# Kernel optimization log

Measured on AMD Instinct MI355X. Metric: run time of the kernel, lower is better.

## Reference

```python
import jax, jax.numpy as jnp
import numpy as np


def setup_inputs() -> dict:
    key = jax.random.key(0)
    ks = jax.random.split(key, 8)
    B, C, H, W = 4, 512, 64, 64
    C8 = C // 8
    return {
        "x": jax.random.normal(ks[0], (B, C, H, W), dtype=jnp.float32),
        "Wq": jax.random.normal(ks[1], (C8, C), dtype=jnp.float32) * 0.02,
        "bq": jax.random.normal(ks[2], (C8,), dtype=jnp.float32) * 0.02,
        "Wk": jax.random.normal(ks[3], (C8, C), dtype=jnp.float32) * 0.02,
        "bk": jax.random.normal(ks[4], (C8,), dtype=jnp.float32) * 0.02,
        "Wv": jax.random.normal(ks[5], (C, C), dtype=jnp.float32) * 0.02,
        "bv": jax.random.normal(ks[6], (C,), dtype=jnp.float32) * 0.02,
        "gamma": jax.random.normal(ks[7], (1,), dtype=jnp.float32),
    }


def reference(x, Wq, bq, Wk, bk, Wv, bv, gamma):
    B, C, H, W = x.shape
    N = H * W
    xf = x.reshape(B, C, N)  # 1x1 conv == per-position matmul over channels
    q = jnp.einsum('oc,bcn->bno', Wq, xf) + bq  # B, N, C//8  (proj_query^T)
    k = jnp.einsum('oc,bcn->bon', Wk, xf) + bk[None, :, None]  # B, C//8, N
    v = jnp.einsum('oc,bcn->bon', Wv, xf) + bv[None, :, None]  # B, C, N
    energy = jnp.einsum('bno,bom->bnm', q, k)  # B, N, N
    attention = jax.nn.softmax(energy, axis=-1)
    # out = bmm(proj_value, attention^T): out[:, :, n] = sum_m v[:, :, m] * att[n, m]
    out = jnp.einsum('bcm,bnm->bcn', v, attention).reshape(B, C, H, W)
    return gamma[0] * out + x
```

## Files before the change

kernel.cpp:

```cpp
#include <hip/hip_runtime.h>
#include <stdint.h>


typedef unsigned short u16;
typedef unsigned char u8;
typedef __attribute__((ext_vector_type(8))) short short8;
typedef __attribute__((ext_vector_type(4))) float f32x4;
typedef __attribute__((ext_vector_type(16))) float f32x16;
typedef __attribute__((ext_vector_type(4))) int i32x4;
typedef __attribute__((ext_vector_type(8))) int i32x8;

#define ASYNC16(gp, lp)                                                        \
  __builtin_amdgcn_global_load_lds(                                            \
      (__attribute__((address_space(1))) void*)(void*)(gp),                    \
      (__attribute__((address_space(3))) void*)(lp), 16, 0, 0)

#define WAIT_VM0 0x0F70
#define WAIT_VM3 0x0F73
#define WAIT_LGKM0 0xC07F

#define EXP_SHIFT 5.0f
#define EXP_CAP 57000.0f

__device__ __forceinline__ u16 f2bf(float f) {
  uint32_t u = __float_as_uint(f);
  u += 0x7FFFu + ((u >> 16) & 1u);
  return (u16)(u >> 16);
}

__device__ __forceinline__ u8 f2fp8(float f) {
  f = fminf(fmaxf(f, -440.f), 440.f);
  int r = __builtin_amdgcn_cvt_pk_fp8_f32(f, f, 0, false);
  return (u8)(r & 0xFF);
}

__global__ __launch_bounds__(256) void k_transpose(const float* __restrict__ x,
                                                   u16* __restrict__ xT) {
  __shared__ float tile[64][65];
  const int b = blockIdx.z;
  const int nb = blockIdx.x * 64;
  const int cb = blockIdx.y * 64;
  const int t = threadIdx.x;
  {
    const int nl = (t & 15) * 4, c0 = t >> 4;
    const float* xp = x + ((size_t)b * 512 + cb) * 4096 + nb;
#pragma unroll
    for (int p = 0; p < 4; ++p) {
      const int cl = c0 + p * 16;
      const float4 v = *(const float4*)(xp + (size_t)cl * 4096 + nl);
      tile[cl][nl] = v.x;
      tile[cl][nl + 1] = v.y;
      tile[cl][nl + 2] = v.z;
      tile[cl][nl + 3] = v.w;
    }
  }
  __syncthreads();
  {
    const int cl = (t & 15) * 4, n0 = t >> 4;
    u16* xtp = xT + ((size_t)b * 4096 + nb) * 512 + cb;
#pragma unroll
    for (int p = 0; p < 4; ++p) {
      const int nl = n0 + p * 16;
      ushort4 o;
      o.x = f2bf(tile[cl][nl]);
      o.y = f2bf(tile[cl + 1][nl]);
      o.z = f2bf(tile[cl + 2][nl]);
      o.w = f2bf(tile[cl + 3][nl]);
      *(ushort4*)(xtp + (size_t)nl * 512 + cl) = o;
    }
  }
}

__global__ __launch_bounds__(256) void k_wcast(const float* __restrict__ Wq,
                                               const float* __restrict__ Wk,
                                               const float* __restrict__ Wv,
                                               u16* __restrict__ wqk,
                                               u16* __restrict__ wv) {
  const int idx = blockIdx.x * 256 + threadIdx.x;
  if (idx < 128 * 512) {
    const int r = idx >> 9, c = idx & 511;
    const float f = (r < 64) ? Wq[r * 512 + c] : Wk[(r - 64) * 512 + c];
    wqk[idx] = f2bf(f);
  } else {
    const int j = idx - 128 * 512;
    if (j < 512 * 512) wv[j] = f2bf(Wv[j]);
  }
}

__device__ __forceinline__ void gemm_bt_tile(const u16* __restrict__ A,
                                             const u16* __restrict__ B,
                                             const int K, const int rowA0,
                                             const int colB0, u16* smem,
                                             f32x4 acc[4][4]) {
  const int t = threadIdx.x;
  const int lane = t & 63, wave = t >> 6;
  const int quad = lane >> 4, l15 = lane & 15;
  const int wr = wave >> 1, wc = wave & 1;
  u16* As = smem;
  u16* Bs = smem + 8192;
  const f32x4 zero = {0.f, 0.f, 0.f, 0.f};
#pragma unroll
  for (int i = 0; i < 4; ++i)
#pragma unroll
    for (int j = 0; j < 4; ++j) acc[i][j] = zero;

  const int srow = t >> 3;
  const int c8 = (lane & 7) ^ (lane >> 3);
  const u16* ga = A + (size_t)(rowA0 + srow) * K + c8 * 8;
  const u16* gb = B + (size_t)(colB0 + srow) * K + c8 * 8;
  char* la = (char*)As + wave * 1024;
  char* lb = (char*)Bs + wave * 1024;
  const size_t rK32 = (size_t)32 * K;

  const int sw0 = (quad) ^ (l15 & 7);
  const int sw1 = (4 + quad) ^ (l15 & 7);

  for (int k0 = 0; k0 < K; k0 += 64) {
    ASYNC16(ga + k0, la);
    ASYNC16(ga + k0 + rK32, la + 4096);
    ASYNC16(ga + k0 + 2 * rK32, la + 8192);
    ASYNC16(ga + k0 + 3 * rK32, la + 12288);
    ASYNC16(gb + k0, lb);
    ASYNC16(gb + k0 + rK32, lb + 4096);
    ASYNC16(gb + k0 + 2 * rK32, lb + 8192);
    ASYNC16(gb + k0 + 3 * rK32, lb + 12288);
    __syncthreads();
#pragma unroll
    for (int s = 0; s < 2; ++s) {
      const int sw = s ? sw1 : sw0;
      short8 a[4], b[4];
#pragma unroll
      for (int i = 0; i < 4; ++i)
        a[i] = *(const short8*)(As + (wr * 64 + i * 16 + l15) * 64 + sw * 8);
#pragma unroll
      for (int j = 0; j < 4; ++j)
        b[j] = *(const short8*)(Bs + (wc * 64 + j * 16 + l15) * 64 + sw * 8);
#pragma unroll
      for (int i = 0; i < 4; ++i)
#pragma unroll
        for (int j = 0; j < 4; ++j)
          acc[i][j] = __builtin_amdgcn_mfma_f32_16x16x32_bf16(a[i], b[j],
                                                              acc[i][j], 0, 0, 0);
    }
    __syncthreads();
  }
}

__global__ __launch_bounds__(256) void k_proj(const u16* __restrict__ xT,
                                              const u16* __restrict__ wqk,
                                              const u16* __restrict__ wv,
                                              const float* __restrict__ bq,
                                              const float* __restrict__ bk,
                                              const float* __restrict__ bv,
                                              u16* __restrict__ q,
                                              u16* __restrict__ kT,
                                              u8* __restrict__ v8) {
  __shared__ u16 smem[16384];
  const int b = blockIdx.z;
  const int by = blockIdx.y;
  const int t = threadIdx.x, lane = t & 63, wave = t >> 6;
  const int quad = lane >> 4, l15 = lane & 15;
  const int wr = wave >> 1, wc = wave & 1;
  f32x4 acc[4][4];

  if (by == 4) {
    const int rowA0 = blockIdx.x * 128;
    gemm_bt_tile(xT + (size_t)b * 4096 * 512, wqk, 512, rowA0, 0, smem, acc);
#pragma unroll
    for (int j = 0; j < 4; ++j) {
      const int col = wc * 64 + j * 16 + l15;
      const float bias = (col < 64) ? bq[col] : bk[col - 64];
#pragma unroll
      for (int i = 0; i < 4; ++i) {
#pragma unroll
        for (int r = 0; r < 4; ++r) {
          const int row = rowA0 + wr * 64 + i * 16 + quad * 4 + r;
          const float val = acc[i][j][r] + bias;
          if (col < 64)
            q[((size_t)b * 4096 + row) * 64 + col] = f2bf(val);
          else
            kT[((size_t)b * 4096 + row) * 64 + (col - 64)] = f2bf(val);
        }
      }
    }
  } else {
    const int rowA0 = by * 128;
    const int colB0 = blockIdx.x * 128;
    gemm_bt_tile(wv, xT + (size_t)b * 4096 * 512, 512, rowA0, colB0, smem, acc);
#pragma unroll
    for (int i = 0; i < 4; ++i) {
#pragma unroll
      for (int r = 0; r < 4; ++r) {
        const int row = rowA0 + wr * 64 + i * 16 + quad * 4 + r;
        const float bias = bv[row];
#pragma unroll
        for (int j = 0; j < 4; ++j) {
          const int col = colB0 + wc * 64 + j * 16 + l15;
          v8[((size_t)b * 512 + row) * 4096 + col] = f2fp8(acc[i][j][r] + bias);
        }
      }
    }
  }
}

__global__ __launch_bounds__(1024, 4) void k_fused(
    const u16* __restrict__ q, const u16* __restrict__ kT,
    const u8* __restrict__ v8, const float* __restrict__ x,
    const float* __restrict__ gamma, float* __restrict__ out) {
  __shared__ u16 k_lds[2][128 * 64];
  __shared__ u8 v_lds[2][2][256 * 64];
  __shared__ u8 P_lds[2][128 * 64];
  __shared__ float lsum_lds[8][128];

  const int t = threadIdx.x;
  const int l = t & 63, w = t >> 6;
  const int quad = l >> 4, l15 = l & 15;
  const int l31 = l & 31, h = l >> 5;

  const int n0 = blockIdx.x * 128;
  const int c0 = blockIdx.y * 256;
  const int b = blockIdx.z;

  const u16* qg = q + ((size_t)b * 4096 + n0) * 64;
  const u16* kg = kT + (size_t)b * 4096 * 64;
  const u8* vg = v8 + ((size_t)b * 512 + c0) * 4096;

  const int kr = t >> 3, kc = t & 7;
  const u16* qsg = qg + kr * 64 + (kc ^ (kr & 7)) * 8;
  const u16* ksg = kg + kr * 64 + (kc ^ (kr & 7)) * 8;
  const int vr = t >> 2, va = t & 3;
  const u8* vsg = vg + (size_t)vr * 4096 + (va ^ ((vr >> 1) & 3)) * 16;

#define STAGE_F(bi, m0)                                                        \
  do {                                                                         \
    ASYNC16(ksg + (size_t)(m0) * 64, (char*)k_lds[bi] + w * 1024);             \
    ASYNC16(vsg + (m0), (char*)v_lds[bi][0] + w * 1024);                       \
    ASYNC16(vsg + (m0) + 64, (char*)v_lds[bi][1] + w * 1024);                  \
  } while (0)

  ASYNC16(qsg, (char*)P_lds[0] + w * 1024);
  STAGE_F(0, 0);
  __builtin_amdgcn_s_waitcnt(WAIT_VM3);
  __builtin_amdgcn_s_barrier();
  asm volatile("" ::: "memory");
  const int ms = w >> 1, nh = w & 1;
  const int sw0 = quad ^ (l15 & 7);
  const int sw1 = (4 + quad) ^ (l15 & 7);
  short8 af[4][2];
#pragma unroll
  for (int s = 0; s < 4; ++s) {
    const u16* qrow = (const u16*)P_lds[0] + (nh * 64 + s * 16 + l15) * 64;
    af[s][0] = *(const short8*)(qrow + sw0 * 8);
    af[s][1] = *(const short8*)(qrow + sw1 * 8);
  }
  asm volatile("" ::: "memory");
  __builtin_amdgcn_s_waitcnt(WAIT_LGKM0);
  __builtin_amdgcn_s_barrier();
  asm volatile("" ::: "memory");

  const int wrp = w >> 2, wcp = w & 3;
  int rowA[2], sA1[2], sA2[2];
#pragma unroll
  for (int i = 0; i < 2; ++i) {
    rowA[i] = wrp * 64 + i * 32 + l31;
    const int fa = (rowA[i] >> 1) & 3;
    sA1[i] = (2 * h) ^ fa;
    sA2[i] = (2 * h + 1) ^ fa;
  }
  const int rowB = wcp * 32 + l31;
  const int fbB = (rowB >> 1) & 3;
  const int sB1 = (2 * h) ^ fbB;
  const int sB2 = (2 * h + 1) ^ fbB;

  const int fbW = (l15 >> 1) & 3;
  u8* Pwbase = P_lds[ms >> 2] + (nh * 64 + l15) * 64 +
               (((ms & 3) ^ fbW) * 16) + quad * 4;

  const int krow_off = (ms * 16 + l15) * 64;

  f32x16 acc[2];
#pragma unroll
  for (int i = 0; i < 2; ++i)
#pragma unroll
    for (int r = 0; r < 16; ++r) acc[i][r] = 0.f;

  float lsums[4] = {0.f, 0.f, 0.f, 0.f};
  const f32x4 zero = {0.f, 0.f, 0.f, 0.f};

  for (int it = 0; it < 32; ++it) {
    __builtin_amdgcn_s_waitcnt(WAIT_VM0);
    asm volatile("" ::: "memory");
    __builtin_amdgcn_s_barrier();
    asm volatile("" ::: "memory");
    const int cur = it & 1;
    if (it + 1 < 32) STAGE_F(cur ^ 1, (it + 1) * 128);

    const u16* kb = k_lds[cur];
    const short8 kf0 = *(const short8*)(kb + krow_off + sw0 * 8);
    const short8 kf1 = *(const short8*)(kb + krow_off + sw1 * 8);
    f32x4 eacc[4];
#pragma unroll
    for (int s = 0; s < 4; ++s) eacc[s] = zero;
    __builtin_amdgcn_s_setprio(1);
#pragma unroll
    for (int s = 0; s < 4; ++s)
      eacc[s] = __builtin_amdgcn_mfma_f32_16x16x32_bf16(kf0, af[s][0],
                                                        eacc[s], 0, 0, 0);
#pragma unroll
    for (int s = 0; s < 4; ++s)
      eacc[s] = __builtin_amdgcn_mfma_f32_16x16x32_bf16(kf1, af[s][1],
                                                        eacc[s], 0, 0, 0);
    __builtin_amdgcn_s_setprio(0);

#pragma unroll
    for (int s = 0; s < 4; ++s) {
      const float e0 = fminf(__expf(eacc[s][0] - EXP_SHIFT), EXP_CAP);
      const float e1 = fminf(__expf(eacc[s][1] - EXP_SHIFT), EXP_CAP);
      const float e2 = fminf(__expf(eacc[s][2] - EXP_SHIFT), EXP_CAP);
      const float e3 = fminf(__expf(eacc[s][3] - EXP_SHIFT), EXP_CAP);
      lsums[s] += (e0 + e1) + (e2 + e3);
      int pk = __builtin_amdgcn_cvt_pk_bf8_f32(e0, e1, 0, false);
      pk = __builtin_amdgcn_cvt_pk_bf8_f32(e2, e3, pk, true);
      *(int*)(Pwbase + s * 1024) = pk;
    }
    asm volatile("" ::: "memory");
    __builtin_amdgcn_s_waitcnt(WAIT_LGKM0);
    __builtin_amdgcn_s_barrier();
    asm volatile("" ::: "memory");

#pragma unroll
    for (int ks = 0; ks < 2; ++ks) {
      const u8* Vb = v_lds[cur][ks];
      const u8* Pb = P_lds[ks];
      i32x8 bb;
      {
        const u8* pb = Pb + rowB * 64;
        const i32x4 blo = *(const i32x4*)(pb + sB1 * 16);
        const i32x4 bhi = *(const i32x4*)(pb + sB2 * 16);
        bb[0] = blo[0]; bb[1] = blo[1]; bb[2] = blo[2]; bb[3] = blo[3];
        bb[4] = bhi[0]; bb[5] = bhi[1]; bb[6] = bhi[2]; bb[7] = bhi[3];
      }
      __builtin_amdgcn_s_setprio(1);
#pragma unroll
      for (int i = 0; i < 2; ++i) {
        const u8* pa = Vb + rowA[i] * 64;
        const i32x4 lo = *(const i32x4*)(pa + sA1[i] * 16);
        const i32x4 hi = *(const i32x4*)(pa + sA2[i] * 16);
        i32x8 a;
        a[0] = lo[0]; a[1] = lo[1]; a[2] = lo[2]; a[3] = lo[3];
        a[4] = hi[0]; a[5] = hi[1]; a[6] = hi[2]; a[7] = hi[3];
        acc[i] = __builtin_amdgcn_mfma_scale_f32_32x32x64_f8f6f4(
            a, bb, acc[i], 0 , 1 , 0, 0x7F, 0, 0x7F);
      }
      __builtin_amdgcn_s_setprio(0);
    }
    asm volatile("" ::: "memory");
  }
#undef STAGE_F

#pragma unroll
  for (int s = 0; s < 4; ++s) {
    lsums[s] += __shfl_xor(lsums[s], 16);
    lsums[s] += __shfl_xor(lsums[s], 32);
  }
  if (l < 16) {
#pragma unroll
    for (int s = 0; s < 4; ++s)
      lsum_lds[ms][nh * 64 + s * 16 + l] = lsums[s];
  }
  asm volatile("" ::: "memory");
  __builtin_amdgcn_s_waitcnt(WAIT_LGKM0);
  __builtin_amdgcn_s_barrier();
  asm volatile("" ::: "memory");

  const float g = gamma[0];
  const int col = n0 + wcp * 32 + l31;
  const int nc = wcp * 32 + l31;
  float den = 0.f;
#pragma unroll
  for (int m = 0; m < 8; ++m) den += lsum_lds[m][nc];
  const float gil = g / den;
#pragma unroll
  for (int i = 0; i < 2; ++i) {
#pragma unroll
    for (int r = 0; r < 16; ++r) {
      const int rloc = (r & 3) + 8 * (r >> 2) + 4 * h;
      const int row = c0 + wrp * 64 + i * 32 + rloc;
      const size_t idx = ((size_t)b * 512 + row) * 4096 + col;
      out[idx] = gil * acc[i][r] + x[idx];
    }
  }
}

extern "C" void kernel_launch(void* const* d_in, const int* in_sizes, int n_in,
                              void* d_out, int out_size, void* d_ws,
                              size_t ws_size, hipStream_t stream) {
  const float* x = (const float*)d_in[0];
  const float* Wq = (const float*)d_in[1];
  const float* bq = (const float*)d_in[2];
  const float* Wk = (const float*)d_in[3];
  const float* bk = (const float*)d_in[4];
  const float* Wv = (const float*)d_in[5];
  const float* bv = (const float*)d_in[6];
  const float* gamma = (const float*)d_in[7];
  float* out = (float*)d_out;

  char* ws = (char*)d_ws;
  u16* xT = (u16*)(ws);
  u16* wqk = (u16*)(ws + 16777216);
  u16* wv = (u16*)(ws + 16908288);
  u16* qb = (u16*)(ws + 17432576);
  u16* ktb = (u16*)(ws + 19529728);
  u8* v8 = (u8*)(ws + 21626880);

  k_transpose<<<dim3(64, 8, 4), 256, 0, stream>>>(x, xT);
  k_wcast<<<dim3(1280), 256, 0, stream>>>(Wq, Wk, Wv, wqk, wv);
  k_proj<<<dim3(32, 5, 4), 256, 0, stream>>>(xT, wqk, wv, bq, bk, bv,
                                             qb, ktb, v8);
  k_fused<<<dim3(32, 2, 4), 1024, 0, stream>>>(qb, ktb, v8, x, gamma, out);
}
```

Baseline: 197.9 us.

## Double-buffer projection GEMM with 8 waves and async prefetch pipeline

The projection GEMM now runs with 512 threads (8 waves, each computing a 64x32 sub-tile) and a two-stage LDS double buffer. The next K-slices are issued with async global-to-LDS loads while MFMAs run on the current buffer, using a vmcnt wait instead of a full sync. MFMA sections are raised to priority 1 with s_setprio. The aim is to hide global load latency and raise occupancy in k_proj, at the cost of twice the LDS per block.

Result: faster. 189.8 us (-4.1%).

```diff
diff --git a/kernel.cpp b/kernel.cpp
--- a/kernel.cpp
+++ b/kernel.cpp
@@ -17,6 +17,7 @@
 
 #define WAIT_VM0 0x0F70
 #define WAIT_VM3 0x0F73
+#define WAIT_VM4 0x0F74
 #define WAIT_LGKM0 0xC07F
 
 #define EXP_SHIFT 5.0f
@@ -87,88 +88,105 @@
   }
 }
 
-__device__ __forceinline__ void gemm_bt_tile(const u16* __restrict__ A,
-                                             const u16* __restrict__ B,
-                                             const int K, const int rowA0,
-                                             const int colB0, u16* smem,
-                                             f32x4 acc[4][4]) {
+__device__ __forceinline__ void gemm8_bt(const u16* __restrict__ A,
+                                         const u16* __restrict__ B,
+                                         const int K, const int rowA0,
+                                         const int colB0, u16* smem,
+                                         f32x4 acc[4][2]) {
   const int t = threadIdx.x;
-  const int lane = t & 63, wave = t >> 6;
+  const int lane = t & 63, w = t >> 6;
   const int quad = lane >> 4, l15 = lane & 15;
-  const int wr = wave >> 1, wc = wave & 1;
-  u16* As = smem;
-  u16* Bs = smem + 8192;
+  const int wr = w >> 2, wc = w & 3;
   const f32x4 zero = {0.f, 0.f, 0.f, 0.f};
 #pragma unroll
   for (int i = 0; i < 4; ++i)
 #pragma unroll
-    for (int j = 0; j < 4; ++j) acc[i][j] = zero;
+    for (int j = 0; j < 2; ++j) acc[i][j] = zero;
 
   const int srow = t >> 3;
   const int c8 = (lane & 7) ^ (lane >> 3);
   const u16* ga = A + (size_t)(rowA0 + srow) * K + c8 * 8;
   const u16* gb = B + (size_t)(colB0 + srow) * K + c8 * 8;
-  char* la = (char*)As + wave * 1024;
-  char* lb = (char*)Bs + wave * 1024;
-  const size_t rK32 = (size_t)32 * K;
+  const size_t rK64 = (size_t)64 * K;
+
+#define STAGE_G(bi, k0)                                                        \
+  do {                                                                         \
+    char* Ab = (char*)smem + (bi) * 32768 + w * 1024;                          \
+    char* Bb = (char*)smem + (bi) * 32768 + 16384 + w * 1024;                  \
+    ASYNC16(ga + (k0), Ab);                                                    \
+    ASYNC16(ga + (k0) + rK64, Ab + 8192);                                      \
+    ASYNC16(gb + (k0), Bb);                                                    \
+    ASYNC16(gb + (k0) + rK64, Bb + 8192);                                      \
+  } while (0)
 
   const int sw0 = (quad) ^ (l15 & 7);
   const int sw1 = (4 + quad) ^ (l15 & 7);
 
-  for (int k0 = 0; k0 < K; k0 += 64) {
-    ASYNC16(ga + k0, la);
-    ASYNC16(ga + k0 + rK32, la + 4096);
-    ASYNC16(ga + k0 + 2 * rK32, la + 8192);
-    ASYNC16(ga + k0 + 3 * rK32, la + 12288);
-    ASYNC16(gb + k0, lb);
-    ASYNC16(gb + k0 + rK32, lb + 4096);
-    ASYNC16(gb + k0 + 2 * rK32, lb + 8192);
-    ASYNC16(gb + k0 + 3 * rK32, lb + 12288);
-    __syncthreads();
+  const int nIt = K >> 6;
+  STAGE_G(0, 0);
+  STAGE_G(1, 64);
+
+  for (int it = 0; it < nIt; ++it) {
+    if (it < nIt - 1)
+      __builtin_amdgcn_s_waitcnt(WAIT_VM4);
+    else
+      __builtin_amdgcn_s_waitcnt(WAIT_VM0);
+    asm volatile("" ::: "memory");
+    __builtin_amdgcn_s_barrier();
+    asm volatile("" ::: "memory");
+
+    const u16* As = smem + (it & 1) * 16384;
+    const u16* Bs = As + 8192;
 #pragma unroll
     for (int s = 0; s < 2; ++s) {
       const int sw = s ? sw1 : sw0;
-      short8 a[4], b[4];
+      short8 a[4], b[2];
 #pragma unroll
       for (int i = 0; i < 4; ++i)
         a[i] = *(const short8*)(As + (wr * 64 + i * 16 + l15) * 64 + sw * 8);
 #pragma unroll
-      for (int j = 0; j < 4; ++j)
-        b[j] = *(const short8*)(Bs + (wc * 64 + j * 16 + l15) * 64 + sw * 8);
+      for (int j = 0; j < 2; ++j)
+        b[j] = *(const short8*)(Bs + (wc * 32 + j * 16 + l15) * 64 + sw * 8);
+      __builtin_amdgcn_s_setprio(1);
 #pragma unroll
       for (int i = 0; i < 4; ++i)
 #pragma unroll
-        for (int j = 0; j < 4; ++j)
+        for (int j = 0; j < 2; ++j)
           acc[i][j] = __builtin_amdgcn_mfma_f32_16x16x32_bf16(a[i], b[j],
                                                               acc[i][j], 0, 0, 0);
-    }
-    __syncthreads();
-  }
-}
-
-__global__ __launch_bounds__(256) void k_proj(const u16* __restrict__ xT,
-                                              const u16* __restrict__ wqk,
-                                              const u16* __restrict__ wv,
-                                              const float* __restrict__ bq,
-                                              const float* __restrict__ bk,
-                                              const float* __restrict__ bv,
-                                              u16* __restrict__ q,
-                                              u16* __restrict__ kT,
-                                              u8* __restrict__ v8) {
-  __shared__ u16 smem[16384];
+      __builtin_amdgcn_s_setprio(0);
+    }
+    asm volatile("" ::: "memory");
+    __builtin_amdgcn_s_barrier();
+    asm volatile("" ::: "memory");
+    if (it + 2 < nIt) STAGE_G(it & 1, (it + 2) * 64);
+  }
+#undef STAGE_G
+}
+
+__global__ __launch_bounds__(512, 4) void k_proj(const u16* __restrict__ xT,
+                                                 const u16* __restrict__ wqk,
+                                                 const u16* __restrict__ wv,
+                                                 const float* __restrict__ bq,
+                                                 const float* __restrict__ bk,
+                                                 const float* __restrict__ bv,
+                                                 u16* __restrict__ q,
+                                                 u16* __restrict__ kT,
+                                                 u8* __restrict__ v8) {
+  __shared__ u16 smem[32768];
   const int b = blockIdx.z;
   const int by = blockIdx.y;
-  const int t = threadIdx.x, lane = t & 63, wave = t >> 6;
+  const int t = threadIdx.x, lane = t & 63, w = t >> 6;
   const int quad = lane >> 4, l15 = lane & 15;
-  const int wr = wave >> 1, wc = wave & 1;
-  f32x4 acc[4][4];
+  const int wr = w >> 2, wc = w & 3;
+  f32x4 acc[4][2];
 
   if (by == 4) {
     const int rowA0 = blockIdx.x * 128;
-    gemm_bt_tile(xT + (size_t)b * 4096 * 512, wqk, 512, rowA0, 0, smem, acc);
-#pragma unroll
-    for (int j = 0; j < 4; ++j) {
-      const int col = wc * 64 + j * 16 + l15;
+    gemm8_bt(xT + (size_t)b * 4096 * 512, wqk, 512, rowA0, 0, smem, acc);
+#pragma unroll
+    for (int j = 0; j < 2; ++j) {
+      const int col = wc * 32 + j * 16 + l15;
       const float bias = (col < 64) ? bq[col] : bk[col - 64];
 #pragma unroll
       for (int i = 0; i < 4; ++i) {
@@ -186,7 +204,7 @@
   } else {
     const int rowA0 = by * 128;
     const int colB0 = blockIdx.x * 128;
-    gemm_bt_tile(wv, xT + (size_t)b * 4096 * 512, 512, rowA0, colB0, smem, acc);
+    gemm8_bt(wv, xT + (size_t)b * 4096 * 512, 512, rowA0, colB0, smem, acc);
 #pragma unroll
     for (int i = 0; i < 4; ++i) {
 #pragma unroll
@@ -194,8 +212,8 @@
         const int row = rowA0 + wr * 64 + i * 16 + quad * 4 + r;
         const float bias = bv[row];
 #pragma unroll
-        for (int j = 0; j < 4; ++j) {
-          const int col = colB0 + wc * 64 + j * 16 + l15;
+        for (int j = 0; j < 2; ++j) {
+          const int col = colB0 + wc * 32 + j * 16 + l15;
           v8[((size_t)b * 512 + row) * 4096 + col] = f2fp8(acc[i][j][r] + bias);
         }
       }
@@ -415,7 +433,7 @@
 
   k_transpose<<<dim3(64, 8, 4), 256, 0, stream>>>(x, xT);
   k_wcast<<<dim3(1280), 256, 0, stream>>>(Wq, Wk, Wv, wqk, wv);
-  k_proj<<<dim3(32, 5, 4), 256, 0, stream>>>(xT, wqk, wv, bq, bk, bv,
+  k_proj<<<dim3(32, 5, 4), 512, 0, stream>>>(xT, wqk, wv, bq, bk, bv,
                                              qb, ktb, v8);
   k_fused<<<dim3(32, 2, 4), 1024, 0, stream>>>(qb, ktb, v8, x, gamma, out);
 }
```
